# Performance work log

Measured on AMD Instinct MI355X. Metric: run time of the kernel, lower is better.

Reference implementation:

```python
import jax, jax.numpy as jnp
import numpy as np

# architecture constants (from __init__)
F = 34          # input frequency bands
K = 7           # rrf_kernel_size
S = 3           # rrf_stride
F_DOWN = (F - K) // S + 1   # 10
C = 64          # hidden_channels
H = F_DOWN * C  # 640
T_MAX = 9       # max_delay (dilated kernel size of Dcls1d)
PAD = (T_MAX - 1) // 2
MS_KS = 200     # minisobel (freq-dependent high-pass exponential) kernel size
W_MS = 0.75
BN_EPS = 1e-5


def setup_inputs() -> dict:
    key = jax.random.key(0)
    ks = jax.random.split(key, 10)
    B, T = 32, 1000
    def g(k, sh, scale):
        return jax.random.normal(k, sh, jnp.float32) * scale
    x = jax.random.normal(ks[0], (B, 1, F, T), jnp.float32)
    # minisobel params: per-frequency EMA coefficient a in (0,1), mixing weight w
    a_vals = jax.random.uniform(ks[1], (F,), jnp.float32, 0.05, 0.5)
    w_vals = jnp.full((F,), W_MS, jnp.float32)
    # DCLS params: one weight + one continuous delay position per synapse
    dcls_w = g(ks[2], (H, 2 * K), 1.0 / np.sqrt(2 * K * T_MAX))
    dcls_p = jax.random.uniform(ks[3], (H, 2 * K), jnp.float32, 0.0, T_MAX - 1.0)
    dcls_b = jnp.zeros((H,), jnp.float32)
    bn_gamma = jnp.ones((C,), jnp.float32)
    bn_beta = jnp.zeros((C,), jnp.float32)
    s = 1.0 / np.sqrt(H)
    W_ih = g(ks[4], (3 * H, H), s)
    W_hh = g(ks[5], (3 * H, H), s)
    b_ih = g(ks[6], (3 * H,), s)
    b_hh = g(ks[7], (3 * H,), s)
    fc_w = g(ks[8], (1, H), s)
    fc_b = jnp.zeros((1,), jnp.float32)
    return dict(x=x, a_vals=a_vals, w_vals=w_vals, dcls_w=dcls_w, dcls_p=dcls_p,
                dcls_b=dcls_b, bn_gamma=bn_gamma, bn_beta=bn_beta,
                W_ih=W_ih, W_hh=W_hh, b_ih=b_ih, b_hh=b_hh, fc_w=fc_w, fc_b=fc_b)


def reference(x, a_vals, w_vals, dcls_w, dcls_p, dcls_b, bn_gamma, bn_beta,
              W_ih, W_hh, b_ih, b_hh, fc_w, fc_b):
    B, T = x.shape[0], x.shape[-1]
    xf = x[:, 0]  # [B,F,T]

    # --- minisobel: per-frequency causal exponential low-pass, high-pass residual,
    #     on/off rectified channels -> [B,2,F,T]
    t_idx = jnp.arange(MS_KS, dtype=x.dtype)
    ema = a_vals[:, None] * (1.0 - a_vals[:, None]) ** t_idx[None, :]  # [F,200]
    ema = ema[:, ::-1][:, None, :]  # flip so correlation = causal convolution
    low = jax.lax.conv_general_dilated(xf, ema, (1,), [(MS_KS - 1, 0)],
                                       dimension_numbers=('NCH', 'OIH', 'NCH'),
                                       feature_group_count=F)
    hp = xf - w_vals[None, :, None] * low
    x2 = jnp.stack([jax.nn.relu(hp), jax.nn.relu(-hp)], axis=1)  # [B,2,F,T]

    # --- unfold over frequency (kernel (K,T), stride (S,1)) + reshape
    #     -> [B, F_down*2*K, T], channels grouped per output frequency band
    rows = jnp.arange(F_DOWN)[:, None] * S + jnp.arange(K)[None, :]  # [F_down,K]
    u = x2[:, :, rows, :]                      # [B,2,F_down,K,T]
    u = u.transpose(0, 2, 1, 3, 4).reshape(B, F_DOWN * 2 * K, T)

    # --- Dcls1d: build interpolated kernel (triangle interpolation of one weight
    #     at a learnable fractional delay), grouped 'same' conv over time
    p = jnp.clip(dcls_p, 0.0, T_MAX - 1.0)     # [H,2K]
    tt = jnp.arange(T_MAX, dtype=x.dtype)
    dk = dcls_w[:, :, None] * jax.nn.relu(1.0 - jnp.abs(tt[None, None, :] - p[:, :, None]))  # [H,2K,T_max]
    y = jax.lax.conv_general_dilated(u, dk, (1,), [(PAD, PAD)],
                                     dimension_numbers=('NCH', 'OIH', 'NCH'),
                                     feature_group_count=F_DOWN)
    y = y + dcls_b[None, :, None]              # [B,H,T]

    # --- [T,B,C,F_down], BatchNorm1d(C) over (T*B, F_down), sigmoid
    y = y.reshape(B, F_DOWN, C, T).transpose(3, 0, 2, 1)  # [T,B,C,F_down]
    mean = y.mean(axis=(0, 1, 3), keepdims=True)
    var = y.var(axis=(0, 1, 3), keepdims=True)
    y = (y - mean) * jax.lax.rsqrt(var + BN_EPS)
    y = jax.nn.sigmoid(y * bn_gamma[None, None, :, None] + 0 + bn_beta[None, None, :, None]) if False else jax.nn.sigmoid(y * bn_gamma[None, None, :, None] + bn_beta[None, None, :, None])

    # --- GRU (torch gate order r,z,n), batch_first output of all hidden states
    seq = y.reshape(T, B, H)
    x_proj = seq @ W_ih.T + b_ih               # [T,B,3H]

    def step(h, xp):
        gh = h @ W_hh.T + b_hh
        xr, xz, xn = jnp.split(xp, 3, axis=-1)
        hr, hz, hn = jnp.split(gh, 3, axis=-1)
        r = jax.nn.sigmoid(xr + hr)
        z = jax.nn.sigmoid(xz + hz)
        n = jnp.tanh(xn + r * hn)
        h = (1.0 - z) * n + z * h
        return h, h

    h0 = jnp.zeros((B, H), x.dtype)
    _, hs = jax.lax.scan(step, h0, x_proj)     # [T,B,H]

    out = hs @ fc_w.T + fc_b                   # [T,B,1]
    return out[..., 0].T                       # [B,T]
```

## Files before the change

kernel.cpp:

```cpp
#include <hip/hip_runtime.h>
#include <hip/hip_fp16.h>
#include <cstdint>

typedef float f4 __attribute__((ext_vector_type(4)));
typedef _Float16 h2v __attribute__((ext_vector_type(2)));
typedef _Float16 half8 __attribute__((ext_vector_type(8)));
typedef unsigned long long u64;


__global__ void k_dk(const float* __restrict__ dcls_w, const float* __restrict__ dcls_p,
                     float* __restrict__ dk) {
    int idx = blockIdx.x * 256 + threadIdx.x;
    if (idx >= 640 * 126) return;
    int h = idx / 126;
    int r = idx % 126;
    int i = r / 9;
    int tau = r % 9;
    float p = dcls_p[h * 14 + i];
    p = fminf(fmaxf(p, 0.f), 8.f);
    float tri = fmaxf(1.f - fabsf((float)tau - p), 0.f);
    dk[idx] = dcls_w[h * 14 + i] * tri;
}

__global__ void k_ema(const float* __restrict__ x, const float* __restrict__ a_vals,
                      const float* __restrict__ w_vals, float* __restrict__ hp) {
    __shared__ float xr[1024];
    int bf = blockIdx.x;
    int f = bf % 34;
    int tid = threadIdx.x;
    const float* xs = x + (size_t)bf * 1000;
    for (int i = tid; i < 1000; i += 256) xr[i] = xs[i];
    for (int i = 1000 + tid; i < 1024; i += 256) xr[i] = 0.f;
    __syncthreads();
    float a = a_vals[f], wv = w_vals[f];
    float om = 1.f - a;
    int t1 = tid, t2 = tid + 256, t3 = tid + 512, t4 = tid + 768;
    bool v4 = (t4 < 1000);
    float a0 = 0.f, a1 = 0.f, a2 = 0.f, a3 = 0.f;
    float coef = a;
    for (int k = 0; k < 200; ++k) {
        a0 += (k <= t1 ? xr[t1 - k] : 0.f) * coef;
        a1 += xr[t2 - k] * coef;
        a2 += xr[t3 - k] * coef;
        a3 += (v4 ? xr[t4 - k] : 0.f) * coef;
        coef *= om;
    }
    float* op = hp + (size_t)bf * 1000;
    op[t1] = xr[t1] - wv * a0;
    op[t2] = xr[t2] - wv * a1;
    op[t3] = xr[t3] - wv * a2;
    if (v4) op[t4] = xr[t4] - wv * a3;
}

__global__ void __launch_bounds__(256) k_conv(const float* __restrict__ hp,
                                              const float* __restrict__ dk,
                                              const float* __restrict__ dcls_b,
                                              float* __restrict__ ybcgt) {
    __shared__ float u[2 * 7 * 264];
    __shared__ float dks[64 * 126];
    int tid = threadIdx.x;
    int t0 = blockIdx.x * 256;
    int g = blockIdx.y;
    int b = blockIdx.z;
    for (int idx = tid; idx < 8064; idx += 256) dks[idx] = dk[g * 8064 + idx];
    for (int idx = tid; idx < 3696; idx += 256) {
        int pm = idx / 1848;
        int rem = idx % 1848;
        int kk = rem / 264;
        int tt = rem % 264;
        int tg = t0 - 4 + tt;
        float v = (tg >= 0 && tg < 1000) ? hp[((size_t)(b * 34 + g * 3 + kk)) * 1000 + tg] : 0.f;
        u[idx] = pm ? fmaxf(-v, 0.f) : fmaxf(v, 0.f);
    }
    __syncthreads();
    int tl = tid & 63;
    int cg4 = tid >> 6;
    float acc[16][4];
#pragma unroll
    for (int ci = 0; ci < 16; ++ci)
#pragma unroll
        for (int tq = 0; tq < 4; ++tq) acc[ci][tq] = 0.f;

    for (int i = 0; i < 14; ++i) {
#pragma unroll
        for (int tau = 0; tau < 9; ++tau) {
            const float* ub = u + i * 264 + tl + tau;
            float u0 = ub[0];
            float u1 = ub[64];
            float u2 = ub[128];
            float u3 = ub[192];
            const float* dp = dks + cg4 * 16 * 126 + i * 9 + tau;
#pragma unroll
            for (int ci = 0; ci < 16; ++ci) {
                float dv = dp[ci * 126];
                acc[ci][0] += u0 * dv;
                acc[ci][1] += u1 * dv;
                acc[ci][2] += u2 * dv;
                acc[ci][3] += u3 * dv;
            }
        }
    }
#pragma unroll
    for (int ci = 0; ci < 16; ++ci) {
        int c = cg4 * 16 + ci;
        float bias = dcls_b[g * 64 + c];
        size_t base = ((size_t)(b * 640 + c * 10 + g)) * 1000;
#pragma unroll
        for (int tq = 0; tq < 4; ++tq) {
            int t = t0 + tq * 64 + tl;
            if (t < 1000) ybcgt[base + t] = acc[ci][tq] + bias;
        }
    }
}

__global__ void k_bnstat(const float* __restrict__ ybcgt, float* __restrict__ bnsum) {
    int c = blockIdx.x / 10;
    int g = blockIdx.x % 10;
    int tid = threadIdx.x;
    float s = 0.f, q = 0.f;
    const float* base = ybcgt + ((size_t)(c * 10 + g)) * 1000;
    for (int b = 0; b < 32; ++b) {
        const float* p = base + (size_t)b * 640000;
        for (int t = tid; t < 1000; t += 256) {
            float v = p[t];
            s += v;
            q += v * v;
        }
    }
    for (int off = 1; off < 64; off <<= 1) {
        s += __shfl_xor(s, off);
        q += __shfl_xor(q, off);
    }
    __shared__ float rs[4], rq[4];
    if ((tid & 63) == 0) { rs[tid >> 6] = s; rq[tid >> 6] = q; }
    __syncthreads();
    if (tid == 0) {
        s = rs[0] + rs[1] + rs[2] + rs[3];
        q = rq[0] + rq[1] + rq[2] + rq[3];
        atomicAdd(&bnsum[c], s);
        atomicAdd(&bnsum[64 + c], q);
    }
}

__global__ void k_bnfin(const float* __restrict__ bnsum, const float* __restrict__ gamma,
                        const float* __restrict__ beta, float* __restrict__ bnp) {
    int c = threadIdx.x;
    const float inv_n = 1.f / 320000.f;
    float mean = bnsum[c] * inv_n;
    float var = bnsum[64 + c] * inv_n - mean * mean;
    float sc = gamma[c] * rsqrtf(var + 1e-5f);
    bnp[c] = sc;
    bnp[64 + c] = beta[c] - mean * sc;
}

__global__ void k_tr(const float* __restrict__ ybcgt, const float* __restrict__ bnp,
                     __half* __restrict__ seq) {
    __shared__ float tile[64 * 65];
    int tid = threadIdx.x;
    int tt0 = blockIdx.x * 64;
    int h0 = blockIdx.y * 64;
    int b = blockIdx.z;
    int tx = tid & 63;
    int ty = tid >> 6;
#pragma unroll
    for (int r = 0; r < 16; ++r) {
        int hh = r * 4 + ty;
        int t = tt0 + tx;
        float v = (t < 1000) ? ybcgt[((size_t)(b * 640 + h0 + hh)) * 1000 + t] : 0.f;
        int c = (h0 + hh) / 10;
        float sarg = bnp[c] * v + bnp[64 + c];
        tile[hh * 65 + tx] = 1.f / (1.f + __expf(-sarg));
    }
    __syncthreads();
#pragma unroll
    for (int r = 0; r < 16; ++r) {
        int t = tt0 + r * 4 + ty;
        if (t < 1000)
            seq[((size_t)t * 32 + b) * 640 + h0 + tx] = __float2half(tile[tx * 65 + r * 4 + ty]);
    }
}

#define BCOL(c) ((c) + (((c) >> 5) << 2))
__global__ void __launch_bounds__(256, 4) k_gemm(const __half* __restrict__ A,
                                                 const float* __restrict__ W,
                                                 const float* __restrict__ bih,
                                                 __half* __restrict__ C) {
    __shared__ float As[8][128];
    __shared__ float Bs[8][140];
    int tid = threadIdx.x;
    int n0 = blockIdx.x * 128;
    int m0 = blockIdx.y * 128;
    int tx = tid & 15;
    int ty = tid >> 4;
    int lm = tid >> 1;
    int lk4 = (tid & 1) * 4;
    int lmB = BCOL(lm);
    const int bc0 = BCOL(tx * 8);
    const int bc1 = BCOL(tx * 8 + 4);
    const __half* Ab = A + (size_t)(m0 + lm) * 640 + lk4;
    const float* Bb = W + (size_t)(n0 + lm) * 640 + lk4;

    f4 c0a = {0,0,0,0}, c0b = {0,0,0,0}, c1a = {0,0,0,0}, c1b = {0,0,0,0};
    f4 c2a = {0,0,0,0}, c2b = {0,0,0,0}, c3a = {0,0,0,0}, c3b = {0,0,0,0};
    f4 c4a = {0,0,0,0}, c4b = {0,0,0,0}, c5a = {0,0,0,0}, c5b = {0,0,0,0};
    f4 c6a = {0,0,0,0}, c6b = {0,0,0,0}, c7a = {0,0,0,0}, c7b = {0,0,0,0};

    for (int kt = 0; kt < 80; ++kt) {
        float2 araw = *(const float2*)(Ab + (size_t)kt * 8);
        const __half2* ah = (const __half2*)&araw;
        float2 a01 = __half22float2(ah[0]);
        float2 a23 = __half22float2(ah[1]);
        float4 bv = *(const float4*)(Bb + (size_t)kt * 8);
        __syncthreads();
        As[lk4 + 0][lm] = a01.x; As[lk4 + 1][lm] = a01.y;
        As[lk4 + 2][lm] = a23.x; As[lk4 + 3][lm] = a23.y;
        Bs[lk4 + 0][lmB] = bv.x; Bs[lk4 + 1][lmB] = bv.y;
        Bs[lk4 + 2][lmB] = bv.z; Bs[lk4 + 3][lmB] = bv.w;
        __syncthreads();
#pragma unroll
        for (int kk = 0; kk < 8; ++kk) {
            f4 blo = *(const f4*)&Bs[kk][bc0];
            f4 bhi = *(const f4*)&Bs[kk][bc1];
            f4 alo = *(const f4*)&As[kk][ty * 8];
            f4 ahi = *(const f4*)&As[kk][ty * 8 + 4];
            c0a += alo.x * blo; c0b += alo.x * bhi;
            c1a += alo.y * blo; c1b += alo.y * bhi;
            c2a += alo.z * blo; c2b += alo.z * bhi;
            c3a += alo.w * blo; c3b += alo.w * bhi;
            c4a += ahi.x * blo; c4b += ahi.x * bhi;
            c5a += ahi.y * blo; c5b += ahi.y * bhi;
            c6a += ahi.z * blo; c6b += ahi.z * bhi;
            c7a += ahi.w * blo; c7b += ahi.w * bhi;
        }
    }
    f4 bblo = *(const f4*)&bih[n0 + tx * 8];
    f4 bbhi = *(const f4*)&bih[n0 + tx * 8 + 4];
    union { __half h[8]; float4 v; } ob;
#define STORE_ROW(i, ra, rb)                                                     \
    {                                                                            \
        f4 lo = ra + bblo; f4 hi = rb + bbhi;                                    \
        ob.h[0] = __float2half(lo.x); ob.h[1] = __float2half(lo.y);              \
        ob.h[2] = __float2half(lo.z); ob.h[3] = __float2half(lo.w);              \
        ob.h[4] = __float2half(hi.x); ob.h[5] = __float2half(hi.y);              \
        ob.h[6] = __float2half(hi.z); ob.h[7] = __float2half(hi.w);              \
        *(float4*)&C[(size_t)(m0 + ty * 8 + i) * 1920 + n0 + tx * 8] = ob.v;     \
    }
    STORE_ROW(0, c0a, c0b) STORE_ROW(1, c1a, c1b) STORE_ROW(2, c2a, c2b)
    STORE_ROW(3, c3a, c3b) STORE_ROW(4, c4a, c4b) STORE_ROW(5, c5a, c5b)
    STORE_ROW(6, c6a, c6b) STORE_ROW(7, c7a, c7b)
#undef STORE_ROW
}

__global__ void __launch_bounds__(512, 1) k_gru(const __half* __restrict__ xp,
                                                const float* __restrict__ Whh,
                                                const float* __restrict__ bhh,
                                                const float* __restrict__ fcw,
                                                u64* __restrict__ slowb,
                                                u64* __restrict__ fastb,
                                                float* __restrict__ fcpart) {
    __shared__ __align__(16) h2v h_lds[16 * 324];
    __shared__ __align__(16) float red[4 * 33 * 4];
    __shared__ float fcred[2][4];

    const int tid = threadIdx.x;
    const int blk = blockIdx.x;
    const int grp = blk & 7;
    const int sl = blk >> 3;
    const int lane = tid & 63;
    const int wid = tid >> 6;

    u64* const sbase = slowb + (size_t)grp * 2560;
    u64* const fbase = fastb + (size_t)grp * 2560;

    const int gte = wid >> 1, jt = wid & 1;
    half8 afrag[20];
    if (wid < 6) {
        int m = lane & 15;
        int kq = lane >> 4;
        const float* wrow = Whh + (size_t)(gte * 640 + sl * 32 + jt * 16 + m) * 640;
#pragma unroll
        for (int s = 0; s < 20; ++s) {
            float4 w0 = *(const float4*)&wrow[s * 32 + kq * 8];
            float4 w1 = *(const float4*)&wrow[s * 32 + kq * 8 + 4];
            afrag[s] = (half8){(_Float16)w0.x, (_Float16)w0.y, (_Float16)w0.z, (_Float16)w0.w,
                               (_Float16)w1.x, (_Float16)w1.y, (_Float16)w1.z, (_Float16)w1.w};
        }
    }
    for (int i = tid; i < 16 * 324; i += 512) h_lds[i] = (h2v){(_Float16)0.f, (_Float16)0.f};

    const int e0 = tid, e1 = tid + 512;
    const bool has3 = (tid < 256);
    const int e2 = has3 ? tid + 1024 : tid;

    const int je = tid >> 2;
    const int be = tid & 3;
    float bh_r = 0.f, bh_z = 0.f, bh_n = 0.f, fw = 0.f, hold = 0.f;
    float xr = 0.f, xz = 0.f, xn = 0.f;
    if (tid < 128) {
        int jg = sl * 32 + je;
        bh_r = bhh[jg];
        bh_z = bhh[640 + jg];
        bh_n = bhh[1280 + jg];
        fw = fcw[jg];
        int bg = grp * 4 + be;
        const __half* xpt = xp + (size_t)bg * 1920;
        xr = __half2float(xpt[jg]);
        xz = __half2float(xpt[640 + jg]);
        xn = __half2float(xpt[1280 + jg]);
    }
    __syncthreads();

    for (int t = 0; t < 1000; ++t) {
        u64* const scur = sbase + (size_t)(t & 1) * 1280;
        u64* const snxt = sbase + (size_t)((t + 1) & 1) * 1280;
        u64* const fcur = fbase + (size_t)(t & 1) * 1280;
        u64* const fnxt = fbase + (size_t)((t + 1) & 1) * 1280;

        u64 v0 = 0, v1 = 0, v2 = 0;
        bool g0 = false, g1 = false, g2 = !has3;
        const unsigned tg = (unsigned)t;
        int round = 0;
        for (;;) {
            u64 f0, f1, f2;
            asm volatile(
                "global_load_dwordx2 %0, %3, off sc0\n\t"
                "global_load_dwordx2 %1, %4, off sc0\n\t"
                "global_load_dwordx2 %2, %5, off sc0\n\t"
                "s_waitcnt vmcnt(0)"
                : "=&v"(f0), "=&v"(f1), "=&v"(f2)
                : "v"(fcur + e0), "v"(fcur + e1), "v"(fcur + e2)
                : "memory");
            if (!g0 && (unsigned)(f0 >> 32) == tg) { v0 = f0; g0 = true; }
            if (!g1 && (unsigned)(f1 >> 32) == tg) { v1 = f1; g1 = true; }
            if (!g2 && (unsigned)(f2 >> 32) == tg) { v2 = f2; g2 = true; }
            if (g0 & g1 & g2) break;
            if ((round & 3) == 2) {
                if (!g0) {
                    u64 s0 = __hip_atomic_load(&scur[e0], __ATOMIC_RELAXED, __HIP_MEMORY_SCOPE_AGENT);
                    if ((unsigned)(s0 >> 32) == tg) { v0 = s0; g0 = true; }
                }
                if (!g1) {
                    u64 s1 = __hip_atomic_load(&scur[e1], __ATOMIC_RELAXED, __HIP_MEMORY_SCOPE_AGENT);
                    if ((unsigned)(s1 >> 32) == tg) { v1 = s1; g1 = true; }
                }
                if (!g2) {
                    u64 s2 = __hip_atomic_load(&scur[e2], __ATOMIC_RELAXED, __HIP_MEMORY_SCOPE_AGENT);
                    if ((unsigned)(s2 >> 32) == tg) { v2 = s2; g2 = true; }
                }
                if (g0 & g1 & g2) break;
            }
            __builtin_amdgcn_s_sleep(1);
            ++round;
        }
        {
            union { unsigned u; h2v h; } pk;
            pk.u = (unsigned)v0; h_lds[(e0 & 3) * 324 + (e0 >> 2)] = pk.h;
            pk.u = (unsigned)v1; h_lds[(e1 & 3) * 324 + (e1 >> 2)] = pk.h;
            if (has3) { pk.u = (unsigned)v2; h_lds[(e2 & 3) * 324 + (e2 >> 2)] = pk.h; }
        }
        __syncthreads();

        float nxr = 0.f, nxz = 0.f, nxn = 0.f;
        if (t + 1 < 1000 && tid < 128) {
            int jg = sl * 32 + je;
            int bg = grp * 4 + be;
            const __half* xpt = xp + ((size_t)(t + 1) * 32 + bg) * 1920;
            nxr = __half2float(xpt[jg]);
            nxz = __half2float(xpt[640 + jg]);
            nxn = __half2float(xpt[1280 + jg]);
        }

        if (wid < 6) {
            int bb = lane & 15;
            int kq = lane >> 4;
            const h2v* hb = &h_lds[bb * 324 + kq * 4];
            f4 acc = {0.f, 0.f, 0.f, 0.f};
#pragma unroll
            for (int s = 0; s < 20; ++s) {
                half8 bfrag = *(const half8*)&hb[s * 16];
                acc = __builtin_amdgcn_mfma_f32_16x16x32_f16(afrag[s], bfrag, acc, 0, 0, 0);
            }
            if (bb < 4) {
#pragma unroll
                for (int i = 0; i < 4; ++i)
                    red[(bb * 33 + jt * 16 + kq * 4 + i) * 4 + gte] = acc[i];
            }
        }
        __syncthreads();

        if (tid < 128) {
            f4 rv = *(const f4*)&red[(be * 33 + je) * 4];
            float hr = bh_r + rv.x;
            float hz = bh_z + rv.y;
            float hn = bh_n + rv.z;
            float r_ = 1.f / (1.f + __expf(-(xr + hr)));
            float z_ = 1.f / (1.f + __expf(-(xz + hz)));
            float pre = xn + r_ * hn;
            float e2v = __expf(-2.f * fabsf(pre));
            float tn = (1.f - e2v) / (1.f + e2v);
            float n_ = (pre >= 0.f) ? tn : -tn;
            float hnew = (1.f - z_) * n_ + z_ * hold;
            hold = hnew;
            float hpair = __shfl_xor(hnew, 4);
            if ((je & 1) == 0) {
                union { h2v h2; unsigned u; } cv;
                cv.h2.x = (_Float16)hnew;
                cv.h2.y = (_Float16)hpair;
                u64 val = (u64)cv.u | ((u64)(unsigned)(t + 1) << 32);
                size_t eo = (size_t)((sl * 16 + (je >> 1)) * 4 + be);
                u64* fp = fnxt + eo;
                asm volatile("global_store_dwordx2 %0, %1, off sc0" :: "v"(fp), "v"(val) : "memory");
                (void)__hip_atomic_exchange(snxt + eo, val,
                                            __ATOMIC_RELAXED, __HIP_MEMORY_SCOPE_AGENT);
            }
            float fv = hnew * fw;
            fv += __shfl_xor(fv, 4);
            fv += __shfl_xor(fv, 8);
            fv += __shfl_xor(fv, 16);
            fv += __shfl_xor(fv, 32);
            if (lane < 4) fcred[wid][lane] = fv;
        }
        xr = nxr; xz = nxz; xn = nxn;
        __syncthreads();
        if (tid < 4)
            fcpart[(size_t)blk * 4000 + t * 4 + tid] = fcred[0][tid] + fcred[1][tid];
    }
}

__global__ void k_fc(const float* __restrict__ fcpart, const float* __restrict__ fcb,
                     float* __restrict__ out) {
    int gid = blockIdx.x * 256 + threadIdx.x;
    int t = gid >> 5;
    int b = gid & 31;
    int g = b >> 2, bi = b & 3;
    float s = fcb[0];
    for (int sl = 0; sl < 20; ++sl)
        s += fcpart[(size_t)(g + 8 * sl) * 4000 + t * 4 + bi];
    out[(size_t)b * 1000 + t] = s;
}

extern "C" void kernel_launch(void* const* d_in, const int* in_sizes, int n_in,
                              void* d_out, int out_size, void* d_ws, size_t ws_size,
                              hipStream_t stream) {
    const float* x      = (const float*)d_in[0];
    const float* a_vals = (const float*)d_in[1];
    const float* w_vals = (const float*)d_in[2];
    const float* dcls_w = (const float*)d_in[3];
    const float* dcls_p = (const float*)d_in[4];
    const float* dcls_b = (const float*)d_in[5];
    const float* gamma  = (const float*)d_in[6];
    const float* beta   = (const float*)d_in[7];
    const float* W_ih   = (const float*)d_in[8];
    const float* W_hh   = (const float*)d_in[9];
    const float* b_ih   = (const float*)d_in[10];
    const float* b_hh   = (const float*)d_in[11];
    const float* fc_w   = (const float*)d_in[12];
    const float* fc_b   = (const float*)d_in[13];
    char* w = (char*)d_ws;

    __half* xpH    = (__half*)(w);
    float* ybcgt   = (float*)(w);
    __half* seqH   = (__half*)(w + 122880000);
    float* hp      = (float*)(w + 122880000);
    float* dk      = (float*)(w + 122880000 + 4352000);
    float* fcpart  = (float*)(w + 122880000);
    u64* fastb     = (u64*)(w + 125440000);
    u64* slowb     = (u64*)(w + 163840000);
    float* bnsum   = (float*)(w + 164003840);

    hipMemsetAsync(w + 163840000, 0, 166912, stream);

    k_dk<<<dim3(315), dim3(256), 0, stream>>>(dcls_w, dcls_p, dk);
    k_ema<<<dim3(1088), dim3(256), 0, stream>>>(x, a_vals, w_vals, hp);
    k_conv<<<dim3(4, 10, 32), dim3(256), 0, stream>>>(hp, dk, dcls_b, ybcgt);
    k_bnstat<<<dim3(640), dim3(256), 0, stream>>>(ybcgt, bnsum);
    k_bnfin<<<dim3(1), dim3(64), 0, stream>>>(bnsum, gamma, beta, (float*)(w + 164004352));
    k_tr<<<dim3(16, 10, 32), dim3(256), 0, stream>>>(ybcgt, (float*)(w + 164004352), seqH);
    k_gemm<<<dim3(15, 250), dim3(256), 0, stream>>>(seqH, W_ih, b_ih, xpH);

    hipMemsetAsync(w + 125440000, 0, 163840, stream);

    {
        const __half* xp_a = xpH;
        void* args[] = {(void*)&xp_a, (void*)&W_hh, (void*)&b_hh, (void*)&fc_w,
                        (void*)&slowb, (void*)&fastb, (void*)&fcpart};
        hipLaunchCooperativeKernel((void*)k_gru, dim3(160), dim3(512), args, 0, stream);
    }

    k_fc<<<dim3(125), dim3(256), 0, stream>>>(fcpart, fc_b, (float*)d_out);
}
```

Measured before the change: 4.148 ms.

## Offload GRU h polling to non-gate warps and lighten barriers

New measurement: 4.402 ms. +6.1%, slower.

```diff
diff --git a/kernel.cpp b/kernel.cpp
--- a/kernel.cpp
+++ b/kernel.cpp
@@ -258,6 +258,7 @@
                                                 u64* __restrict__ slowb,
                                                 u64* __restrict__ fastb,
                                                 float* __restrict__ fcpart) {
+#define BARRIER() asm volatile("s_waitcnt lgkmcnt(0)\n\ts_barrier" ::: "memory")
     __shared__ __align__(16) h2v h_lds[16 * 324];
     __shared__ __align__(16) float red[4 * 33 * 4];
     __shared__ float fcred[2][4];
@@ -288,9 +289,10 @@
     }
     for (int i = tid; i < 16 * 324; i += 512) h_lds[i] = (h2v){(_Float16)0.f, (_Float16)0.f};
 
-    const int e0 = tid, e1 = tid + 512;
-    const bool has3 = (tid < 256);
-    const int e2 = has3 ? tid + 1024 : tid;
+    const int tp = tid - 128;
+    const int E0 = tp, E1 = tp + 384, E2 = tp + 768;
+    const bool h4 = (tp < 128);
+    const int E3 = (tid >= 128 && h4) ? (1152 + tp) : E0;
 
     const int je = tid >> 2;
     const int be = tid & 3;
@@ -316,49 +318,56 @@
         u64* const fcur = fbase + (size_t)(t & 1) * 1280;
         u64* const fnxt = fbase + (size_t)((t + 1) & 1) * 1280;
 
-        u64 v0 = 0, v1 = 0, v2 = 0;
-        bool g0 = false, g1 = false, g2 = !has3;
-        const unsigned tg = (unsigned)t;
-        int round = 0;
-        for (;;) {
-            u64 f0, f1, f2;
-            asm volatile(
-                "global_load_dwordx2 %0, %3, off sc0\n\t"
-                "global_load_dwordx2 %1, %4, off sc0\n\t"
-                "global_load_dwordx2 %2, %5, off sc0\n\t"
-                "s_waitcnt vmcnt(0)"
-                : "=&v"(f0), "=&v"(f1), "=&v"(f2)
-                : "v"(fcur + e0), "v"(fcur + e1), "v"(fcur + e2)
-                : "memory");
-            if (!g0 && (unsigned)(f0 >> 32) == tg) { v0 = f0; g0 = true; }
-            if (!g1 && (unsigned)(f1 >> 32) == tg) { v1 = f1; g1 = true; }
-            if (!g2 && (unsigned)(f2 >> 32) == tg) { v2 = f2; g2 = true; }
-            if (g0 & g1 & g2) break;
-            if ((round & 3) == 2) {
-                if (!g0) {
-                    u64 s0 = __hip_atomic_load(&scur[e0], __ATOMIC_RELAXED, __HIP_MEMORY_SCOPE_AGENT);
-                    if ((unsigned)(s0 >> 32) == tg) { v0 = s0; g0 = true; }
+        if (tid >= 128) {
+            u64 v0 = 0, v1 = 0, v2 = 0, v3 = 0;
+            bool g0 = false, g1 = false, g2 = false, g3 = !h4;
+            const unsigned tg = (unsigned)t;
+            int round = 0;
+            for (;;) {
+                u64 f0, f1, f2, f3;
+                asm volatile(
+                    "global_load_dwordx2 %0, %4, off sc0\n\t"
+                    "global_load_dwordx2 %1, %5, off sc0\n\t"
+                    "global_load_dwordx2 %2, %6, off sc0\n\t"
+                    "global_load_dwordx2 %3, %7, off sc0\n\t"
+                    "s_waitcnt vmcnt(0)"
+                    : "=&v"(f0), "=&v"(f1), "=&v"(f2), "=&v"(f3)
+                    : "v"(fcur + E0), "v"(fcur + E1), "v"(fcur + E2), "v"(fcur + E3)
+                    : "memory");
+                if (!g0 && (unsigned)(f0 >> 32) == tg) { v0 = f0; g0 = true; }
+                if (!g1 && (unsigned)(f1 >> 32) == tg) { v1 = f1; g1 = true; }
+                if (!g2 && (unsigned)(f2 >> 32) == tg) { v2 = f2; g2 = true; }
+                if (!g3 && (unsigned)(f3 >> 32) == tg) { v3 = f3; g3 = true; }
+                if (g0 & g1 & g2 & g3) break;
+                if ((round & 3) == 2) {
+                    if (!g0) {
+                        u64 s0 = __hip_atomic_load(&scur[E0], __ATOMIC_RELAXED, __HIP_MEMORY_SCOPE_AGENT);
+                        if ((unsigned)(s0 >> 32) == tg) { v0 = s0; g0 = true; }
+                    }
+                    if (!g1) {
+                        u64 s1 = __hip_atomic_load(&scur[E1], __ATOMIC_RELAXED, __HIP_MEMORY_SCOPE_AGENT);
+                        if ((unsigned)(s1 >> 32) == tg) { v1 = s1; g1 = true; }
+                    }
+                    if (!g2) {
+                        u64 s2 = __hip_atomic_load(&scur[E2], __ATOMIC_RELAXED, __HIP_MEMORY_SCOPE_AGENT);
+                        if ((unsigned)(s2 >> 32) == tg) { v2 = s2; g2 = true; }
+                    }
+                    if (!g3) {
+                        u64 s3 = __hip_atomic_load(&scur[E3], __ATOMIC_RELAXED, __HIP_MEMORY_SCOPE_AGENT);
+                        if ((unsigned)(s3 >> 32) == tg) { v3 = s3; g3 = true; }
+                    }
+                    if (g0 & g1 & g2 & g3) break;
                 }
-                if (!g1) {
-                    u64 s1 = __hip_atomic_load(&scur[e1], __ATOMIC_RELAXED, __HIP_MEMORY_SCOPE_AGENT);
-                    if ((unsigned)(s1 >> 32) == tg) { v1 = s1; g1 = true; }
-                }
-                if (!g2) {
-                    u64 s2 = __hip_atomic_load(&scur[e2], __ATOMIC_RELAXED, __HIP_MEMORY_SCOPE_AGENT);
-                    if ((unsigned)(s2 >> 32) == tg) { v2 = s2; g2 = true; }
-                }
-                if (g0 & g1 & g2) break;
+                __builtin_amdgcn_s_sleep(1);
+                ++round;
             }
-            __builtin_amdgcn_s_sleep(1);
-            ++round;
-        }
-        {
             union { unsigned u; h2v h; } pk;
-            pk.u = (unsigned)v0; h_lds[(e0 & 3) * 324 + (e0 >> 2)] = pk.h;
-            pk.u = (unsigned)v1; h_lds[(e1 & 3) * 324 + (e1 >> 2)] = pk.h;
-            if (has3) { pk.u = (unsigned)v2; h_lds[(e2 & 3) * 324 + (e2 >> 2)] = pk.h; }
-        }
-        __syncthreads();
+            pk.u = (unsigned)v0; h_lds[(E0 & 3) * 324 + (E0 >> 2)] = pk.h;
+            pk.u = (unsigned)v1; h_lds[(E1 & 3) * 324 + (E1 >> 2)] = pk.h;
+            pk.u = (unsigned)v2; h_lds[(E2 & 3) * 324 + (E2 >> 2)] = pk.h;
+            if (h4) { pk.u = (unsigned)v3; h_lds[(E3 & 3) * 324 + (E3 >> 2)] = pk.h; }
+        }
+        BARRIER();
 
         float nxr = 0.f, nxz = 0.f, nxn = 0.f;
         if (t + 1 < 1000 && tid < 128) {
@@ -386,7 +395,7 @@
                     red[(bb * 33 + jt * 16 + kq * 4 + i) * 4 + gte] = acc[i];
             }
         }
-        __syncthreads();
+        BARRIER();
 
         if (tid < 128) {
             f4 rv = *(const f4*)&red[(be * 33 + je) * 4];
@@ -410,8 +419,8 @@
                 size_t eo = (size_t)((sl * 16 + (je >> 1)) * 4 + be);
                 u64* fp = fnxt + eo;
                 asm volatile("global_store_dwordx2 %0, %1, off sc0" :: "v"(fp), "v"(val) : "memory");
-                (void)__hip_atomic_exchange(snxt + eo, val,
-                                            __ATOMIC_RELAXED, __HIP_MEMORY_SCOPE_AGENT);
+                __hip_atomic_store(snxt + eo, val,
+                                   __ATOMIC_RELAXED, __HIP_MEMORY_SCOPE_AGENT);
             }
             float fv = hnew * fw;
             fv += __shfl_xor(fv, 4);
@@ -421,10 +430,11 @@
             if (lane < 4) fcred[wid][lane] = fv;
         }
         xr = nxr; xz = nxz; xn = nxn;
-        __syncthreads();
+        BARRIER();
         if (tid < 4)
             fcpart[(size_t)blk * 4000 + t * 4 + tid] = fcred[0][tid] + fcred[1][tid];
     }
+#undef BARRIER
 }
 
 __global__ void k_fc(const float* __restrict__ fcpart, const float* __restrict__ fcb,
```

## Rewrite input-projection GEMM to use fp16 MFMA 16x16x32 instructions

Applied to the files above, without the earlier changes.

After: 3.451 ms. -16.8%, faster.

```diff
diff --git a/kernel.cpp b/kernel.cpp
--- a/kernel.cpp
+++ b/kernel.cpp
@@ -180,75 +180,77 @@
     }
 }
 
-#define BCOL(c) ((c) + (((c) >> 5) << 2))
-__global__ void __launch_bounds__(256, 4) k_gemm(const __half* __restrict__ A,
+__global__ void __launch_bounds__(256, 2) k_gemm(const __half* __restrict__ A,
                                                  const float* __restrict__ W,
                                                  const float* __restrict__ bih,
                                                  __half* __restrict__ C) {
-    __shared__ float As[8][128];
-    __shared__ float Bs[8][140];
-    int tid = threadIdx.x;
-    int n0 = blockIdx.x * 128;
-    int m0 = blockIdx.y * 128;
-    int tx = tid & 15;
-    int ty = tid >> 4;
-    int lm = tid >> 1;
-    int lk4 = (tid & 1) * 4;
-    int lmB = BCOL(lm);
-    const int bc0 = BCOL(tx * 8);
-    const int bc1 = BCOL(tx * 8 + 4);
-    const __half* Ab = A + (size_t)(m0 + lm) * 640 + lk4;
-    const float* Bb = W + (size_t)(n0 + lm) * 640 + lk4;
-
-    f4 c0a = {0,0,0,0}, c0b = {0,0,0,0}, c1a = {0,0,0,0}, c1b = {0,0,0,0};
-    f4 c2a = {0,0,0,0}, c2b = {0,0,0,0}, c3a = {0,0,0,0}, c3b = {0,0,0,0};
-    f4 c4a = {0,0,0,0}, c4b = {0,0,0,0}, c5a = {0,0,0,0}, c5b = {0,0,0,0};
-    f4 c6a = {0,0,0,0}, c6b = {0,0,0,0}, c7a = {0,0,0,0}, c7b = {0,0,0,0};
-
-    for (int kt = 0; kt < 80; ++kt) {
-        float2 araw = *(const float2*)(Ab + (size_t)kt * 8);
-        const __half2* ah = (const __half2*)&araw;
-        float2 a01 = __half22float2(ah[0]);
-        float2 a23 = __half22float2(ah[1]);
-        float4 bv = *(const float4*)(Bb + (size_t)kt * 8);
+    __shared__ __align__(16) _Float16 As[128 * 40];
+    __shared__ __align__(16) _Float16 Bs[128 * 40];
+    const int tid = threadIdx.x;
+    const int n0 = blockIdx.x * 128;
+    const int m0 = blockIdx.y * 128;
+    const int lane = tid & 63;
+    const int wid = tid >> 6;
+    const int ml = lane & 15;
+    const int kq = lane >> 4;
+    const int wm = (wid & 1) * 64;
+    const int wn = (wid >> 1) * 64;
+    const int sr = tid >> 1;
+    const int sc = (tid & 1) * 16;
+
+    f4 acc[4][4];
+#pragma unroll
+    for (int mt = 0; mt < 4; ++mt)
+#pragma unroll
+        for (int nt = 0; nt < 4; ++nt) acc[mt][nt] = (f4){0.f, 0.f, 0.f, 0.f};
+
+    const __half* Ag = A + (size_t)(m0 + sr) * 640 + sc;
+    const float* Wg = W + (size_t)(n0 + sr) * 640 + sc;
+
+    for (int s = 0; s < 20; ++s) {
+        const int k0 = s * 32;
+        half8 a0 = *(const half8*)(Ag + k0);
+        half8 a1 = *(const half8*)(Ag + k0 + 8);
+        float4 b0 = *(const float4*)(Wg + k0);
+        float4 b1 = *(const float4*)(Wg + k0 + 4);
+        float4 b2 = *(const float4*)(Wg + k0 + 8);
+        float4 b3 = *(const float4*)(Wg + k0 + 12);
         __syncthreads();
-        As[lk4 + 0][lm] = a01.x; As[lk4 + 1][lm] = a01.y;
-        As[lk4 + 2][lm] = a23.x; As[lk4 + 3][lm] = a23.y;
-        Bs[lk4 + 0][lmB] = bv.x; Bs[lk4 + 1][lmB] = bv.y;
-        Bs[lk4 + 2][lmB] = bv.z; Bs[lk4 + 3][lmB] = bv.w;
+        *(half8*)&As[sr * 40 + sc] = a0;
+        *(half8*)&As[sr * 40 + sc + 8] = a1;
+        half8 bh0 = {(_Float16)b0.x, (_Float16)b0.y, (_Float16)b0.z, (_Float16)b0.w,
+                     (_Float16)b1.x, (_Float16)b1.y, (_Float16)b1.z, (_Float16)b1.w};
+        half8 bh1 = {(_Float16)b2.x, (_Float16)b2.y, (_Float16)b2.z, (_Float16)b2.w,
+                     (_Float16)b3.x, (_Float16)b3.y, (_Float16)b3.z, (_Float16)b3.w};
+        *(half8*)&Bs[sr * 40 + sc] = bh0;
+        *(half8*)&Bs[sr * 40 + sc + 8] = bh1;
         __syncthreads();
-#pragma unroll
-        for (int kk = 0; kk < 8; ++kk) {
-            f4 blo = *(const f4*)&Bs[kk][bc0];
-            f4 bhi = *(const f4*)&Bs[kk][bc1];
-            f4 alo = *(const f4*)&As[kk][ty * 8];
-            f4 ahi = *(const f4*)&As[kk][ty * 8 + 4];
-            c0a += alo.x * blo; c0b += alo.x * bhi;
-            c1a += alo.y * blo; c1b += alo.y * bhi;
-            c2a += alo.z * blo; c2b += alo.z * bhi;
-            c3a += alo.w * blo; c3b += alo.w * bhi;
-            c4a += ahi.x * blo; c4b += ahi.x * bhi;
-            c5a += ahi.y * blo; c5b += ahi.y * bhi;
-            c6a += ahi.z * blo; c6b += ahi.z * bhi;
-            c7a += ahi.w * blo; c7b += ahi.w * bhi;
-        }
-    }
-    f4 bblo = *(const f4*)&bih[n0 + tx * 8];
-    f4 bbhi = *(const f4*)&bih[n0 + tx * 8 + 4];
-    union { __half h[8]; float4 v; } ob;
-#define STORE_ROW(i, ra, rb)                                                     \
-    {                                                                            \
-        f4 lo = ra + bblo; f4 hi = rb + bbhi;                                    \
-        ob.h[0] = __float2half(lo.x); ob.h[1] = __float2half(lo.y);              \
-        ob.h[2] = __float2half(lo.z); ob.h[3] = __float2half(lo.w);              \
-        ob.h[4] = __float2half(hi.x); ob.h[5] = __float2half(hi.y);              \
-        ob.h[6] = __float2half(hi.z); ob.h[7] = __float2half(hi.w);              \
-        *(float4*)&C[(size_t)(m0 + ty * 8 + i) * 1920 + n0 + tx * 8] = ob.v;     \
-    }
-    STORE_ROW(0, c0a, c0b) STORE_ROW(1, c1a, c1b) STORE_ROW(2, c2a, c2b)
-    STORE_ROW(3, c3a, c3b) STORE_ROW(4, c4a, c4b) STORE_ROW(5, c5a, c5b)
-    STORE_ROW(6, c6a, c6b) STORE_ROW(7, c7a, c7b)
-#undef STORE_ROW
+        half8 af[4], bf[4];
+#pragma unroll
+        for (int mt = 0; mt < 4; ++mt)
+            af[mt] = *(const half8*)&As[(wm + mt * 16 + ml) * 40 + kq * 8];
+#pragma unroll
+        for (int nt = 0; nt < 4; ++nt)
+            bf[nt] = *(const half8*)&Bs[(wn + nt * 16 + ml) * 40 + kq * 8];
+#pragma unroll
+        for (int mt = 0; mt < 4; ++mt)
+#pragma unroll
+            for (int nt = 0; nt < 4; ++nt)
+                acc[mt][nt] = __builtin_amdgcn_mfma_f32_16x16x32_f16(af[mt], bf[nt],
+                                                                     acc[mt][nt], 0, 0, 0);
+    }
+#pragma unroll
+    for (int nt = 0; nt < 4; ++nt) {
+        int n = n0 + wn + nt * 16 + ml;
+        float bias = bih[n];
+#pragma unroll
+        for (int mt = 0; mt < 4; ++mt) {
+            int mbase = m0 + wm + mt * 16 + kq * 4;
+#pragma unroll
+            for (int i = 0; i < 4; ++i)
+                C[(size_t)(mbase + i) * 1920 + n] = __float2half(acc[mt][nt][i] + bias);
+        }
+    }
 }
 
 __global__ void __launch_bounds__(512, 1) k_gru(const __half* __restrict__ xp,
```
